# Performance work log

Measured on AMD Instinct MI355X. Metric: run time of the kernel, lower is better.

## Reference

```python
import jax, jax.numpy as jnp
import numpy as np

DEPTH = 128
NEG_MAX = -jnp.finfo(jnp.float32).max


def setup_inputs() -> dict:
    key = jax.random.key(0)
    ks = jax.random.split(key, 10)
    B, S, F, C = 16, 2048, 512, 1000
    x = jax.random.normal(ks[0], (B, S, F), dtype=jnp.float32)
    attention_mask = jax.random.randint(ks[1], (B, S, S), 0, 2) == 1
    s = 1.0 / np.sqrt(F)
    Wq = jax.random.uniform(ks[2], (F, DEPTH), jnp.float32, -s, s)
    bq = jax.random.uniform(ks[3], (DEPTH,), jnp.float32, -s, s)
    Wk = jax.random.uniform(ks[4], (F, DEPTH), jnp.float32, -s, s)
    bk = jax.random.uniform(ks[5], (DEPTH,), jnp.float32, -s, s)
    Wv = jax.random.uniform(ks[6], (F, DEPTH), jnp.float32, -s, s)
    bv = jax.random.uniform(ks[7], (DEPTH,), jnp.float32, -s, s)
    sl = 1.0 / np.sqrt(DEPTH)
    Wl = jax.random.uniform(ks[8], (DEPTH, C), jnp.float32, -sl, sl)
    bl = jax.random.uniform(ks[9], (C,), jnp.float32, -sl, sl)
    return {"x": x, "attention_mask": attention_mask,
            "Wq": Wq, "bq": bq, "Wk": Wk, "bk": bk,
            "Wv": Wv, "bv": bv, "Wl": Wl, "bl": bl}


def reference(x, attention_mask, Wq, bq, Wk, bk, Wv, bv, Wl, bl):
    # x: [B, S, F]; single-head attention with depth=128
    q = (x @ Wq + bq) * (DEPTH ** -0.5)          # [B, S, D] (is_scaled_dot_product)
    k = x @ Wk + bk                               # [B, S, D]
    v = x @ Wv + bv                               # [B, S, D]
    logit = jnp.einsum('bsd,btd->bst', q, k)      # [B, S, S]
    # masked_fill_(mask, -float_max) then added to logits
    logit = logit + jnp.where(attention_mask, NEG_MAX, 0.0)
    attn = jax.nn.softmax(logit, axis=2)
    out = jnp.einsum('bst,btd->bsd', attn, v)     # [B, S, D]
    out = out @ Wl + bl                           # [B, S, C]
    return out.mean(axis=1)                       # [B, C]
```

## Files before the change

kernel.cpp:

```cpp
#include <hip/hip_runtime.h>
#include <stdint.h>

#define BB 16
#define SS 2048
#define FF 512
#define DD 128
#define CC 1000

typedef __attribute__((ext_vector_type(8))) short bf16x8;
typedef __attribute__((ext_vector_type(4))) float f32x4;

__device__ __forceinline__ unsigned short f2bf(float f) {
  unsigned x;
  __builtin_memcpy(&x, &f, 4);
  x = x + 0x7FFFu + ((x >> 16) & 1u);
  return (unsigned short)(x >> 16);
}
__device__ __forceinline__ float bf2f(unsigned short u) {
  unsigned x = ((unsigned)u) << 16;
  float f;
  __builtin_memcpy(&f, &x, 4);
  return f;
}
__device__ __forceinline__ unsigned pk2(float a, float b) {
  return (unsigned)f2bf(a) | ((unsigned)f2bf(b) << 16);
}

#define WS_PK   0
#define WS_Q    8388608
#define WS_K    16777216
#define WS_V    25165824
#define WS_WT   33554432
#define WS_WGP  33947648
#define WS_END  42336256

__global__ __launch_bounds__(256) void k_prep(const void* __restrict__ mask,
                                              const float* __restrict__ Wq,
                                              const float* __restrict__ Wk,
                                              const float* __restrict__ Wv,
                                              unsigned short* __restrict__ wt,
                                              unsigned* __restrict__ pk) {
  __shared__ unsigned red;
  const int tid = threadIdx.x;
  if (tid == 0) red = 0;
  __syncthreads();
  {
    unsigned a = 0;
    const unsigned* m32 = (const unsigned*)mask;
#pragma unroll
    for (int j = 0; j < 4; ++j) a |= m32[tid * 4 + j] & 0xFFFFFF00u;
    if (a) atomicOr(&red, 1u);
  }
  __syncthreads();
  const bool isInt = (red == 0);

  const long long base = (long long)blockIdx.x * 32768;
  for (int it = 0; it < 128; ++it) {
    long long e = base + it * 256 + tid;
    int val;
    if (isInt) val = ((const int*)mask)[e];
    else       val = ((const unsigned char*)mask)[e];
    unsigned long long bal = __ballot(val != 0);
    if ((tid & 31) == 0)
      pk[e >> 5] = (unsigned)((tid & 63) ? (bal >> 32) : bal);
  }

  if (blockIdx.x < 768) {
    int idx = blockIdx.x * 256 + tid;
    int ty = idx >> 16;
    int o = idx & 65535;
    int d = o >> 9, f = o & 511;
    const float* W = ty == 0 ? Wq : (ty == 1 ? Wk : Wv);
    wt[idx] = f2bf(W[f * DD + d]);
  }
}

__global__ __launch_bounds__(256) void k_proj(const float* __restrict__ xg,
                                              const unsigned short* __restrict__ wtg,
                                              const float* __restrict__ bq,
                                              const float* __restrict__ bk,
                                              const float* __restrict__ bv,
                                              unsigned short* __restrict__ qo,
                                              unsigned short* __restrict__ ko,
                                              unsigned short* __restrict__ vo) {
  extern __shared__ __align__(16) char smem[];
  char* xA = smem;
  char* lB = smem + 131072;
  const int tid = threadIdx.x;
  const int lane = tid & 63;
  const int wv = tid >> 6;
  const int colL = lane & 15, quad = lane >> 4;
  const int blk = blockIdx.x;
  const int m0 = (wv & 1) * 64, n0 = (wv >> 1) * 64;

#pragma unroll 4
  for (int it = 0; it < 32; ++it) {
    int id = it * 256 + tid;
    int row = id >> 6, c = id & 63;
    const float* xp = xg + (size_t)(blk * 128 + row) * FF + c * 8;
    float4 x0 = *(const float4*)xp;
    float4 x1 = *(const float4*)(xp + 4);
    uint4 w;
    w.x = pk2(x0.x, x0.y); w.y = pk2(x0.z, x0.w);
    w.z = pk2(x1.x, x1.y); w.w = pk2(x1.z, x1.w);
    *(uint4*)(xA + row * 1024 + (c ^ (row & 63)) * 16) = w;
  }

  for (int ty = 0; ty < 3; ++ty) {
    const float* bias = ty == 0 ? bq : (ty == 1 ? bk : bv);
    unsigned short* outp = ty == 0 ? qo : (ty == 1 ? ko : vo);
    const float scale = ty == 0 ? 0.08838834764831845f : 1.0f;
    const unsigned short* wbase = wtg + (size_t)ty * 65536;

    f32x4 acc[4][4];
    const f32x4 z4 = {0.f, 0.f, 0.f, 0.f};
#pragma unroll
    for (int mi = 0; mi < 4; ++mi)
#pragma unroll
      for (int ni = 0; ni < 4; ++ni) acc[mi][ni] = z4;

    for (int ic = 0; ic < 16; ++ic) {
      const int k0 = ic * 32;
      uint4 vb[2];
#pragma unroll
      for (int rr = 0; rr < 2; ++rr) {
        int p = rr * 256 + tid;
        int row = p >> 2, c = p & 3;
        vb[rr] = *(const uint4*)(wbase + (size_t)row * FF + k0 + c * 8);
      }
      __syncthreads();
#pragma unroll
      for (int rr = 0; rr < 2; ++rr) {
        int p = rr * 256 + tid;
        int row = p >> 2, c = p & 3;
        int phys = c ^ ((row >> 1) & 3);
        *(uint4*)(lB + row * 64 + phys * 16) = vb[rr];
      }
      __syncthreads();
      bf16x8 af[4], bfr[4];
#pragma unroll
      for (int mi = 0; mi < 4; ++mi) {
        int ar = m0 + mi * 16 + colL;
        int cch = ic * 4 + quad;
        int phys = cch ^ (ar & 63);
        af[mi] = *(const bf16x8*)(xA + ar * 1024 + phys * 16);
      }
#pragma unroll
      for (int ni = 0; ni < 4; ++ni) {
        int br = n0 + ni * 16 + colL;
        int phys = quad ^ ((br >> 1) & 3);
        bfr[ni] = *(const bf16x8*)(lB + br * 64 + phys * 16);
      }
#pragma unroll
      for (int mi = 0; mi < 4; ++mi)
#pragma unroll
        for (int ni = 0; ni < 4; ++ni)
          acc[mi][ni] = __builtin_amdgcn_mfma_f32_16x16x32_bf16(af[mi], bfr[ni], acc[mi][ni], 0, 0, 0);
    }
#pragma unroll
    for (int ni = 0; ni < 4; ++ni) {
      int col = n0 + ni * 16 + colL;
      float bval = bias[col];
#pragma unroll
      for (int mi = 0; mi < 4; ++mi) {
#pragma unroll
        for (int r = 0; r < 4; ++r) {
          int row = blk * 128 + m0 + mi * 16 + quad * 4 + r;
          float val = (acc[mi][ni][r] + bval) * scale;
          outp[(size_t)row * DD + col] = f2bf(val);
        }
      }
    }
  }
}

__global__ __launch_bounds__(512, 2) void k_fatt(const unsigned short* __restrict__ qg,
                                                 const unsigned short* __restrict__ kg,
                                                 const unsigned* __restrict__ pk,
                                                 float* __restrict__ wgp) {
  __shared__ __align__(16) char kt[32768];
  __shared__ unsigned mk[32 * 65];
  __shared__ float wacc[2048];
  __shared__ float zfin[32];
  __shared__ float zinvl[32];

  const int tid = threadIdx.x;
  const int lane = tid & 63, wv = tid >> 6;
  const int colL = lane & 15, quad = lane >> 4;
  const int wr = wv & 1, wq = wv >> 1;
  const int r0 = blockIdx.x * 32;
  const int b = blockIdx.y;

  for (int i = tid; i < 2048; i += 512) {
    int row = i >> 6, w = i & 63;
    mk[row * 65 + w] = pk[((size_t)b * SS + r0 + row) * 64 + w];
    wacc[i] = 0.f;
  }
  if (tid < 32) zfin[tid] = 0.f;

  bf16x8 qf[4];
  {
    int qrow = r0 + wr * 16 + colL;
    const unsigned short* qp = qg + ((size_t)b * SS + qrow) * DD + quad * 8;
#pragma unroll
    for (int kk = 0; kk < 4; ++kk) qf[kk] = *(const bf16x8*)(qp + kk * 32);
  }

  const int krow = tid >> 3, kc8 = tid & 7;
  const unsigned short* kbase = kg + ((size_t)b * SS + krow) * DD;
  const int kswz0 = (kc8 ^ (krow & 7)) * 16;
  const int kswz1 = ((kc8 + 8) ^ (krow & 7)) * 16;

  {
    uint4 k0r = *(const uint4*)(kbase + kc8 * 8);
    uint4 k1r = *(const uint4*)(kbase + kc8 * 8 + 64);
    *(uint4*)(kt + krow * 256 + kswz0) = k0r;
    *(uint4*)(kt + krow * 256 + kswz1) = k1r;
  }
  __syncthreads();

  float z[4] = {0.f, 0.f, 0.f, 0.f};
  unsigned estore[64];
  const int tb = wq * 16 + colL;

#pragma unroll
  for (int c = 0; c < 32; ++c) {
    uint4 k0r, k1r;
    if (c < 31) {
      const unsigned short* kb2 = kbase + (size_t)(c + 1) * 64 * DD;
      k0r = *(const uint4*)(kb2 + kc8 * 8);
      k1r = *(const uint4*)(kb2 + kc8 * 8 + 64);
    }
    const char* ktb = kt + (c & 1) * 16384;
    bf16x8 bb[4];
#pragma unroll
    for (int kk = 0; kk < 4; ++kk) {
      int phys = (kk * 4 + quad) ^ (tb & 7);
      bb[kk] = *(const bf16x8*)(ktb + tb * 256 + phys * 16);
    }
    f32x4 acc = {0.f, 0.f, 0.f, 0.f};
    acc = __builtin_amdgcn_mfma_f32_16x16x32_bf16(qf[0], bb[0], acc, 0, 0, 0);
    acc = __builtin_amdgcn_mfma_f32_16x16x32_bf16(qf[1], bb[1], acc, 0, 0, 0);
    acc = __builtin_amdgcn_mfma_f32_16x16x32_bf16(qf[2], bb[2], acc, 0, 0, 0);
    acc = __builtin_amdgcn_mfma_f32_16x16x32_bf16(qf[3], bb[3], acc, 0, 0, 0);
    const int tl = c * 64 + tb;
    const int widx = tl >> 5, wb = tl & 31;
    const int rbase = wr * 16 + quad * 4;
    float e0, e1, e2, e3;
    {
      unsigned mw0 = mk[(rbase + 0) * 65 + widx];
      unsigned mw1 = mk[(rbase + 1) * 65 + widx];
      unsigned mw2 = mk[(rbase + 2) * 65 + widx];
      unsigned mw3 = mk[(rbase + 3) * 65 + widx];
      e0 = ((mw0 >> wb) & 1u) ? 0.f : __expf(fminf(acc[0], 80.f));
      e1 = ((mw1 >> wb) & 1u) ? 0.f : __expf(fminf(acc[1], 80.f));
      e2 = ((mw2 >> wb) & 1u) ? 0.f : __expf(fminf(acc[2], 80.f));
      e3 = ((mw3 >> wb) & 1u) ? 0.f : __expf(fminf(acc[3], 80.f));
    }
    z[0] += e0; z[1] += e1; z[2] += e2; z[3] += e3;
    estore[c * 2]     = pk2(e0, e1);
    estore[c * 2 + 1] = pk2(e2, e3);
    if (c < 31) {
      char* ktn = kt + ((c + 1) & 1) * 16384;
      *(uint4*)(ktn + krow * 256 + kswz0) = k0r;
      *(uint4*)(ktn + krow * 256 + kswz1) = k1r;
      __syncthreads();
    }
  }

#pragma unroll
  for (int r = 0; r < 4; ++r) {
    float s = z[r];
    s += __shfl_xor(s, 1, 64);
    s += __shfl_xor(s, 2, 64);
    s += __shfl_xor(s, 4, 64);
    s += __shfl_xor(s, 8, 64);
    if (colL == 0) atomicAdd(&zfin[wr * 16 + quad * 4 + r], s);
  }
  __syncthreads();
  if (tid < 32) zinvl[tid] = 1.0f / fmaxf(zfin[tid], 1e-30f);
  __syncthreads();

  {
    f32x4 zi = *(const f32x4*)(zinvl + wr * 16 + quad * 4);
#pragma unroll
    for (int c = 0; c < 32; ++c) {
      unsigned u0 = estore[c * 2], u1 = estore[c * 2 + 1];
      float cs = bf2f((unsigned short)(u0 & 0xFFFFu)) * zi[0]
               + bf2f((unsigned short)(u0 >> 16))     * zi[1]
               + bf2f((unsigned short)(u1 & 0xFFFFu)) * zi[2]
               + bf2f((unsigned short)(u1 >> 16))     * zi[3];
      cs += __shfl_xor(cs, 16, 64);
      cs += __shfl_xor(cs, 32, 64);
      if (quad == 0) atomicAdd(&wacc[c * 64 + wq * 16 + colL], cs);
    }
  }
  __syncthreads();
  {
    const int t0 = tid * 4;
    float4 o4;
    o4.x = wacc[t0]; o4.y = wacc[t0 + 1]; o4.z = wacc[t0 + 2]; o4.w = wacc[t0 + 3];
    *(float4*)(wgp + ((size_t)b * 64 + blockIdx.x) * SS + t0) = o4;
  }
}

__global__ __launch_bounds__(1024) void k_tail(const float* __restrict__ wgp,
                                               const unsigned short* __restrict__ vg,
                                               const float* __restrict__ Wl,
                                               const float* __restrict__ bl,
                                               float* __restrict__ outp) {
  __shared__ float ws2[2048];
  __shared__ float yp[8][128];
  __shared__ float ys[128];
  const int tid = threadIdx.x;
  const int b = blockIdx.x;

  {
    float s0 = 0.f, s1 = 0.f;
    const float* wp = wgp + ((size_t)b * 64) * SS + tid * 2;
#pragma unroll 8
    for (int rg = 0; rg < 64; ++rg) {
      s0 += wp[rg * SS];
      s1 += wp[rg * SS + 1];
    }
    ws2[tid * 2] = s0;
    ws2[tid * 2 + 1] = s1;
  }
  __syncthreads();

  {
    const int d = tid & 127, tg = tid >> 7;
    const int t0 = tg * 256;
    float p = 0.f;
    const unsigned short* vr = vg + ((size_t)b * SS + t0) * DD + d;
#pragma unroll 8
    for (int t = 0; t < 256; ++t) p += ws2[t0 + t] * bf2f(vr[(size_t)t * DD]);
    yp[tg][d] = p;
  }
  __syncthreads();
  if (tid < 128) {
    float a = 0.f;
#pragma unroll
    for (int g = 0; g < 8; ++g) a += yp[g][tid];
    ys[tid] = a * (1.0f / 2048.0f);
  }
  __syncthreads();

  if (tid < CC) {
    float a = bl[tid];
#pragma unroll 16
    for (int dd = 0; dd < DD; ++dd) a += ys[dd] * Wl[dd * CC + tid];
    outp[b * CC + tid] = a;
  }
}

extern "C" void kernel_launch(void* const* d_in, const int* in_sizes, int n_in,
                              void* d_out, int out_size, void* d_ws, size_t ws_size,
                              hipStream_t stream) {
  const void* ptr[10];
  for (int i = 0; i < 10; ++i) ptr[i] = (i < n_in) ? d_in[i] : nullptr;
  if (n_in == 10) {
    const void *px = 0, *pm = 0, *pWl = 0, *pbl = 0;
    const void* pW[3] = {0, 0, 0};
    const void* pb[3] = {0, 0, 0};
    int nW = 0, nb = 0;
    for (int i = 0; i < 10; ++i) {
      int s = in_sizes[i];
      if (s == 16777216) px = d_in[i];
      else if (s == 67108864) pm = d_in[i];
      else if (s == 128000) pWl = d_in[i];
      else if (s == 1000) pbl = d_in[i];
      else if (s == 65536 && nW < 3) pW[nW++] = d_in[i];
      else if (s == 128 && nb < 3) pb[nb++] = d_in[i];
    }
    if (px && pm && pWl && pbl && nW == 3 && nb == 3) {
      ptr[0] = px; ptr[1] = pm;
      ptr[2] = pW[0]; ptr[3] = pb[0];
      ptr[4] = pW[1]; ptr[5] = pb[1];
      ptr[6] = pW[2]; ptr[7] = pb[2];
      ptr[8] = pWl; ptr[9] = pbl;
    }
  }
  char* ws = (char*)d_ws;
  if (ws_size < (size_t)WS_END) return;
  unsigned* pk = (unsigned*)(ws + WS_PK);
  unsigned short* q  = (unsigned short*)(ws + WS_Q);
  unsigned short* k  = (unsigned short*)(ws + WS_K);
  unsigned short* v  = (unsigned short*)(ws + WS_V);
  unsigned short* wt = (unsigned short*)(ws + WS_WT);
  float* wgp = (float*)(ws + WS_WGP);

  k_prep<<<2048, 256, 0, stream>>>(ptr[1], (const float*)ptr[2], (const float*)ptr[4],
                                   (const float*)ptr[6], wt, pk);
  k_proj<<<256, 256, 139264, stream>>>((const float*)ptr[0], wt,
                                       (const float*)ptr[3], (const float*)ptr[5],
                                       (const float*)ptr[7], q, k, v);
  k_fatt<<<dim3(64, 16), 512, 0, stream>>>(q, k, pk, wgp);
  k_tail<<<16, 1024, 0, stream>>>(wgp, v, (const float*)ptr[8], (const float*)ptr[9],
                                  (float*)d_out);
}
```

Baseline: 625.3 us.

## Split QKV projection across grid y and stream x tiles through small LDS

The projection kernel now launches one block per (row tile, Q/K/V) pair instead of looping over the three projections inside each block. Instead of staging a 128x512 bf16 x tile in 128KB of dynamic LDS, each block streams 32-wide K-chunks of x into an 8KB LDS buffer alongside the weight chunk. This triples the block count and greatly cuts LDS use, which raises occupancy. In exchange, x is read from global memory and converted to bf16 three times.

```diff
diff --git a/kernel.cpp b/kernel.cpp
--- a/kernel.cpp
+++ b/kernel.cpp
@@ -83,92 +83,80 @@
                                               unsigned short* __restrict__ qo,
                                               unsigned short* __restrict__ ko,
                                               unsigned short* __restrict__ vo) {
-  extern __shared__ __align__(16) char smem[];
-  char* xA = smem;
-  char* lB = smem + 131072;
+  __shared__ __align__(16) char lA[8192];
+  __shared__ __align__(16) char lB[8192];
   const int tid = threadIdx.x;
   const int lane = tid & 63;
   const int wv = tid >> 6;
   const int colL = lane & 15, quad = lane >> 4;
-  const int blk = blockIdx.x;
+  const int blk = blockIdx.x, ty = blockIdx.y;
+  const float* bias = ty == 0 ? bq : (ty == 1 ? bk : bv);
+  unsigned short* outp = ty == 0 ? qo : (ty == 1 ? ko : vo);
+  const float scale = ty == 0 ? 0.08838834764831845f : 1.0f;
+  const unsigned short* wbase = wtg + (size_t)ty * 65536;
   const int m0 = (wv & 1) * 64, n0 = (wv >> 1) * 64;
 
-#pragma unroll 4
-  for (int it = 0; it < 32; ++it) {
-    int id = it * 256 + tid;
-    int row = id >> 6, c = id & 63;
-    const float* xp = xg + (size_t)(blk * 128 + row) * FF + c * 8;
-    float4 x0 = *(const float4*)xp;
-    float4 x1 = *(const float4*)(xp + 4);
-    uint4 w;
-    w.x = pk2(x0.x, x0.y); w.y = pk2(x0.z, x0.w);
-    w.z = pk2(x1.x, x1.y); w.w = pk2(x1.z, x1.w);
-    *(uint4*)(xA + row * 1024 + (c ^ (row & 63)) * 16) = w;
-  }
-
-  for (int ty = 0; ty < 3; ++ty) {
-    const float* bias = ty == 0 ? bq : (ty == 1 ? bk : bv);
-    unsigned short* outp = ty == 0 ? qo : (ty == 1 ? ko : vo);
-    const float scale = ty == 0 ? 0.08838834764831845f : 1.0f;
-    const unsigned short* wbase = wtg + (size_t)ty * 65536;
-
-    f32x4 acc[4][4];
-    const f32x4 z4 = {0.f, 0.f, 0.f, 0.f};
+  f32x4 acc[4][4];
+  const f32x4 z4 = {0.f, 0.f, 0.f, 0.f};
+#pragma unroll
+  for (int mi = 0; mi < 4; ++mi)
+#pragma unroll
+    for (int ni = 0; ni < 4; ++ni) acc[mi][ni] = z4;
+
+  for (int ic = 0; ic < 16; ++ic) {
+    const int k0 = ic * 32;
+    uint4 va[2], vb[2];
+#pragma unroll
+    for (int rr = 0; rr < 2; ++rr) {
+      int p = rr * 256 + tid;
+      int row = p >> 2, c = p & 3;
+      const float* xp = xg + (size_t)(blk * 128 + row) * FF + k0 + c * 8;
+      float4 x0 = *(const float4*)xp;
+      float4 x1 = *(const float4*)(xp + 4);
+      va[rr].x = pk2(x0.x, x0.y); va[rr].y = pk2(x0.z, x0.w);
+      va[rr].z = pk2(x1.x, x1.y); va[rr].w = pk2(x1.z, x1.w);
+      vb[rr] = *(const uint4*)(wbase + (size_t)row * FF + k0 + c * 8);
+    }
+    __syncthreads();
+#pragma unroll
+    for (int rr = 0; rr < 2; ++rr) {
+      int p = rr * 256 + tid;
+      int row = p >> 2, c = p & 3;
+      int phys = c ^ ((row >> 1) & 3);
+      *(uint4*)(lA + row * 64 + phys * 16) = va[rr];
+      *(uint4*)(lB + row * 64 + phys * 16) = vb[rr];
+    }
+    __syncthreads();
+    bf16x8 af[4], bfr[4];
+#pragma unroll
+    for (int mi = 0; mi < 4; ++mi) {
+      int ar = m0 + mi * 16 + colL;
+      int phys = quad ^ ((ar >> 1) & 3);
+      af[mi] = *(const bf16x8*)(lA + ar * 64 + phys * 16);
+    }
+#pragma unroll
+    for (int ni = 0; ni < 4; ++ni) {
+      int br = n0 + ni * 16 + colL;
+      int phys = quad ^ ((br >> 1) & 3);
+      bfr[ni] = *(const bf16x8*)(lB + br * 64 + phys * 16);
+    }
 #pragma unroll
     for (int mi = 0; mi < 4; ++mi)
 #pragma unroll
-      for (int ni = 0; ni < 4; ++ni) acc[mi][ni] = z4;
-
-    for (int ic = 0; ic < 16; ++ic) {
-      const int k0 = ic * 32;
-      uint4 vb[2];
-#pragma unroll
-      for (int rr = 0; rr < 2; ++rr) {
-        int p = rr * 256 + tid;
-        int row = p >> 2, c = p & 3;
-        vb[rr] = *(const uint4*)(wbase + (size_t)row * FF + k0 + c * 8);
-      }
-      __syncthreads();
-#pragma unroll
-      for (int rr = 0; rr < 2; ++rr) {
-        int p = rr * 256 + tid;
-        int row = p >> 2, c = p & 3;
-        int phys = c ^ ((row >> 1) & 3);
-        *(uint4*)(lB + row * 64 + phys * 16) = vb[rr];
-      }
-      __syncthreads();
-      bf16x8 af[4], bfr[4];
-#pragma unroll
-      for (int mi = 0; mi < 4; ++mi) {
-        int ar = m0 + mi * 16 + colL;
-        int cch = ic * 4 + quad;
-        int phys = cch ^ (ar & 63);
-        af[mi] = *(const bf16x8*)(xA + ar * 1024 + phys * 16);
-      }
-#pragma unroll
-      for (int ni = 0; ni < 4; ++ni) {
-        int br = n0 + ni * 16 + colL;
-        int phys = quad ^ ((br >> 1) & 3);
-        bfr[ni] = *(const bf16x8*)(lB + br * 64 + phys * 16);
-      }
-#pragma unroll
-      for (int mi = 0; mi < 4; ++mi)
-#pragma unroll
-        for (int ni = 0; ni < 4; ++ni)
-          acc[mi][ni] = __builtin_amdgcn_mfma_f32_16x16x32_bf16(af[mi], bfr[ni], acc[mi][ni], 0, 0, 0);
-    }
-#pragma unroll
-    for (int ni = 0; ni < 4; ++ni) {
-      int col = n0 + ni * 16 + colL;
-      float bval = bias[col];
-#pragma unroll
-      for (int mi = 0; mi < 4; ++mi) {
-#pragma unroll
-        for (int r = 0; r < 4; ++r) {
-          int row = blk * 128 + m0 + mi * 16 + quad * 4 + r;
-          float val = (acc[mi][ni][r] + bval) * scale;
-          outp[(size_t)row * DD + col] = f2bf(val);
-        }
+      for (int ni = 0; ni < 4; ++ni)
+        acc[mi][ni] = __builtin_amdgcn_mfma_f32_16x16x32_bf16(af[mi], bfr[ni], acc[mi][ni], 0, 0, 0);
+  }
+#pragma unroll
+  for (int ni = 0; ni < 4; ++ni) {
+    int col = n0 + ni * 16 + colL;
+    float bval = bias[col];
+#pragma unroll
+    for (int mi = 0; mi < 4; ++mi) {
+#pragma unroll
+      for (int r = 0; r < 4; ++r) {
+        int row = blk * 128 + m0 + mi * 16 + quad * 4 + r;
+        float val = (acc[mi][ni][r] + bval) * scale;
+        outp[(size_t)row * DD + col] = f2bf(val);
       }
     }
   }
@@ -392,9 +380,9 @@
 
   k_prep<<<2048, 256, 0, stream>>>(ptr[1], (const float*)ptr[2], (const float*)ptr[4],
                                    (const float*)ptr[6], wt, pk);
-  k_proj<<<256, 256, 139264, stream>>>((const float*)ptr[0], wt,
-                                       (const float*)ptr[3], (const float*)ptr[5],
-                                       (const float*)ptr[7], q, k, v);
+  k_proj<<<dim3(256, 3), 256, 0, stream>>>((const float*)ptr[0], wt,
+                                           (const float*)ptr[3], (const float*)ptr[5],
+                                           (const float*)ptr[7], q, k, v);
   k_fatt<<<dim3(64, 16), 512, 0, stream>>>(q, k, pk, wgp);
   k_tail<<<16, 1024, 0, stream>>>(wgp, v, (const float*)ptr[8], (const float*)ptr[9],
                                   (float*)d_out);
```

Measured after the change: 611.3 us. -2.2%, faster.
